# Kernel tuning notes

Measured on AMD Instinct MI355X. Metric: run time of the kernel, lower is better.

## Reference

```python
import jax, jax.numpy as jnp
import numpy as np

DEPTH, EMBED, HEADS, FF = 4, 512, 8, 2048
POS_SCALE, POS_WEIGHT = 0.1, 1.0
EPS = 1e-5  # torch LayerNorm default


def setup_inputs() -> dict:
    key = jax.random.key(0)
    ks = jax.random.split(key, 6)
    B, L = 8, 1024
    s = 0.02
    x = jax.random.normal(ks[0], (B, L, EMBED), jnp.float32)
    Wqkv = jax.random.normal(ks[1], (DEPTH, 3 * EMBED, EMBED), jnp.float32) * s
    bqkv = jnp.zeros((DEPTH, 3 * EMBED), jnp.float32)
    W1 = jax.random.normal(ks[2], (DEPTH, FF, EMBED), jnp.float32) * s
    b1 = jnp.zeros((DEPTH, FF), jnp.float32)
    W2 = jax.random.normal(ks[3], (DEPTH, EMBED, FF), jnp.float32) * s
    b2 = jnp.zeros((DEPTH, EMBED), jnp.float32)
    g = jnp.ones((DEPTH, EMBED), jnp.float32)
    bt = jnp.zeros((DEPTH, EMBED), jnp.float32)
    return {"input": x, "Wqkv": Wqkv, "bqkv": bqkv, "W1": W1, "b1": b1,
            "W2": W2, "b2": b2, "g1": g, "bt1": bt, "g2": g, "bt2": bt,
            "g3": g, "bt3": bt}


def _ln(x, g, b):
    m = x.mean(-1, keepdims=True)
    v = ((x - m) ** 2).mean(-1, keepdims=True)
    return (x - m) * jax.lax.rsqrt(v + EPS) * g + b


def reference(input, Wqkv, bqkv, W1, b1, W2, b2, g1, bt1, g2, bt2, g3, bt3):
    x = input
    B, L, E = x.shape
    hd = E // HEADS
    pos_idx = jnp.arange(L)
    # additive relative-position bias: exp(-|i-j| * scale) * weight
    pos = jnp.exp(-jnp.abs(pos_idx[:, None] - pos_idx[None, :]).astype(x.dtype) * POS_SCALE) * POS_WEIGHT
    triu = jnp.triu(jnp.ones((L, L), dtype=bool), 1)
    inv_sqrt_hd = jnp.asarray(1.0 / np.sqrt(hd), x.dtype)
    for d in range(DEPTH):
        # --- RelativeMultiheadAttention self-attn block ---
        qkv = jnp.einsum('ble,fe->blf', x, Wqkv[d]) + bqkv[d]
        q = qkv[..., :E].reshape(B, L, HEADS, hd).transpose(0, 2, 1, 3)
        k = qkv[..., E:2 * E].reshape(B, L, HEADS, hd).transpose(0, 2, 1, 3)
        logits = jnp.einsum('bhqd,bhkd->bhqk', q, k) * inv_sqrt_hd
        # nn.MultiheadAttention returns head-AVERAGED softmax weights
        A = jax.nn.softmax(logits, axis=-1).mean(axis=1)  # [B,L,L]
        # torch: attn_logits[triu(attn_logits,1).to(bool)] = -inf (nonzero strict upper)
        A = jnp.where(triu & (A != 0), -jnp.inf, A)
        W = jax.nn.softmax(A + pos[None], axis=-1)
        sa = jnp.einsum('bqk,bke->bqe', W, x)  # value is RAW x (no v-proj/out-proj)
        x = _ln(x + sa, g1[d], bt1[d])
        # --- NoopAttention cross-attn block contributes zeros ---
        x = _ln(x, g2[d], bt2[d])
        # --- FFN block (relu activation, post-norm) ---
        h = jax.nn.relu(jnp.einsum('ble,fe->blf', x, W1[d]) + b1[d])
        ff = jnp.einsum('blf,ef->ble', h, W2[d]) + b2[d]
        x = _ln(x + ff, g3[d], bt3[d])
    return x
```

## Files before the change

### kernel.cpp

```cpp
#include <hip/hip_runtime.h>

#define NB 8
#define SEQ 1024
#define EMB 512
#define FFD 2048
#define NROWS (NB*SEQ)
#define LNEPS 1e-5f

typedef __bf16 bf16x8 __attribute__((ext_vector_type(8)));
typedef float f32x4 __attribute__((ext_vector_type(4)));

__device__ __forceinline__ unsigned short f2bf(float f){
  unsigned u = __builtin_bit_cast(unsigned, f);
  u += 0x7fffu + ((u>>16)&1u);
  return (unsigned short)(u>>16);
}
__device__ __forceinline__ bf16x8 ld_bf8(const unsigned short* p){
  return *(const bf16x8*)p;
}
__device__ __forceinline__ void async_copy16(const void* g, void* l){
  __builtin_amdgcn_global_load_lds((const __attribute__((address_space(1))) unsigned int*)g,
                                   (__attribute__((address_space(3))) unsigned int*)l,
                                   16, 0, 0);
}

__device__ __forceinline__ float2 block_sum2(float a,float b){
  #pragma unroll
  for(int k=32;k>=1;k>>=1){ a += __shfl_xor(a,k,64); b += __shfl_xor(b,k,64); }
  __shared__ float sa[4], sb[4];
  int w = threadIdx.x>>6;
  __syncthreads();
  if((threadIdx.x&63)==0){ sa[w]=a; sb[w]=b; }
  __syncthreads();
  return make_float2(sa[0]+sa[1]+sa[2]+sa[3], sb[0]+sb[1]+sb[2]+sb[3]);
}

template<bool OUTBF16, bool RELU, bool BIAS, bool CAUSAL, int NT>
__global__ __launch_bounds__(256,4) void gemm_db(
    const unsigned short* __restrict__ Ag, const unsigned short* __restrict__ Bg,
    const float* __restrict__ bias, void* __restrict__ Cg,
    int K, int lda, int ldb, int ldc,
    long long strA, long long strB, long long strC)
{
  constexpr int NJ = NT/32;
  __shared__ unsigned short As[2][128*32];
  __shared__ unsigned short Bs[2][NT*32];
  const unsigned short* Ab = Ag + blockIdx.z*strA;
  const unsigned short* Bb = Bg + blockIdx.z*strB;
  const int m0 = blockIdx.y*128, n0 = blockIdx.x*NT;
  const int t = threadIdx.x;
  const int lane = t & 63, w = t >> 6;
  const int wy = w >> 1, wx = w & 1;
  const int q = lane >> 4, c = lane & 15;
  f32x4 acc[4][NJ] = {};
  const int kend = CAUSAL ? (m0 + 128) : K;
  const int srow = t >> 2;
  const int sk = (t & 3) * 8;
  const int gk = ((t & 3) ^ ((t >> 3) & 3)) * 8;
  const int rs = (q ^ ((c >> 1) & 3)) * 8;

#define STAGE(bi, kk) do { \
    async_copy16(Ab + (long long)(m0 + srow)*lda + (kk) + gk,      &As[bi][srow*32 + sk]); \
    async_copy16(Ab + (long long)(m0 + srow + 64)*lda + (kk) + gk, &As[bi][(srow+64)*32 + sk]); \
    async_copy16(Bb + (long long)(n0 + srow)*ldb + (kk) + gk,      &Bs[bi][srow*32 + sk]); \
    if(NT == 128) \
      async_copy16(Bb + (long long)(n0 + srow + 64)*ldb + (kk) + gk, &Bs[bi][(srow+64)*32 + sk]); \
  } while(0)

  STAGE(0, 0);
  int buf = 0;
  for(int k0 = 0; k0 < kend; k0 += 32, buf ^= 1){
    __syncthreads();
    if(k0 + 32 < kend) STAGE(buf^1, k0 + 32);
    bf16x8 af[4], bfr[NJ];
    #pragma unroll
    for(int fi=0; fi<4; fi++) af[fi]  = ld_bf8(&As[buf][(wy*64 + fi*16 + c)*32 + rs]);
    #pragma unroll
    for(int fj=0; fj<NJ; fj++) bfr[fj] = ld_bf8(&Bs[buf][(wx*(NT/2) + fj*16 + c)*32 + rs]);
    #pragma unroll
    for(int fi=0; fi<4; fi++)
      #pragma unroll
      for(int fj=0; fj<NJ; fj++)
        acc[fi][fj] = __builtin_amdgcn_mfma_f32_16x16x32_bf16(af[fi], bfr[fj], acc[fi][fj], 0,0,0);
  }
#undef STAGE
  #pragma unroll
  for(int fi=0; fi<4; fi++){
    #pragma unroll
    for(int fj=0; fj<NJ; fj++){
      const int row = m0 + wy*64 + fi*16 + q*4;
      const int col = n0 + wx*(NT/2) + fj*16 + c;
      const float bv = (BIAS && blockIdx.z==0) ? bias[col] : 0.f;
      #pragma unroll
      for(int r=0; r<4; r++){
        float v = acc[fi][fj][r] + bv;
        if(RELU) v = fmaxf(v, 0.f);
        long long off = blockIdx.z*strC + (long long)(row+r)*ldc + col;
        if(OUTBF16) ((unsigned short*)Cg)[off] = f2bf(v);
        else        ((float*)Cg)[off] = v;
      }
    }
  }
}

__global__ __launch_bounds__(256) void qk_dsum(
    const unsigned short* __restrict__ qkv, float* __restrict__ dsum)
{
  __shared__ unsigned short As[128*32];
  __shared__ unsigned short Bs[128*32];
  const int bh = blockIdx.z, b = bh >> 3, h = bh & 7;
  const int i0 = blockIdx.y*128, j0 = blockIdx.x*128;
  const unsigned short* Ab = qkv + (long long)b*SEQ*1024 + h*64;
  const unsigned short* Bb = qkv + (long long)b*SEQ*1024 + 512 + h*64;
  const int t = threadIdx.x, lane = t & 63, w = t >> 6;
  const int wy = w >> 1, wx = w & 1, q = lane >> 4, c = lane & 15;
  f32x4 acc[4][4] = {};
  const int srow = t >> 2;
  const int sk = (t & 3) * 8;
  const int gk = ((t & 3) ^ ((t >> 3) & 3)) * 8;
  const int rs = (q ^ ((c >> 1) & 3)) * 8;
  #pragma unroll
  for(int k0 = 0; k0 < 64; k0 += 32){
    async_copy16(Ab + (long long)(i0 + srow)*1024 + k0 + gk,      As + srow*32 + sk);
    async_copy16(Ab + (long long)(i0 + srow + 64)*1024 + k0 + gk, As + (srow+64)*32 + sk);
    async_copy16(Bb + (long long)(j0 + srow)*1024 + k0 + gk,      Bs + srow*32 + sk);
    async_copy16(Bb + (long long)(j0 + srow + 64)*1024 + k0 + gk, Bs + (srow+64)*32 + sk);
    __syncthreads();
    bf16x8 af[4], bfr[4];
    #pragma unroll
    for(int fi=0; fi<4; fi++) af[fi]  = ld_bf8(As + (wy*64 + fi*16 + c)*32 + rs);
    #pragma unroll
    for(int fj=0; fj<4; fj++) bfr[fj] = ld_bf8(Bs + (wx*64 + fj*16 + c)*32 + rs);
    #pragma unroll
    for(int fi=0; fi<4; fi++)
      #pragma unroll
      for(int fj=0; fj<4; fj++)
        acc[fi][fj] = __builtin_amdgcn_mfma_f32_16x16x32_bf16(af[fi], bfr[fj], acc[fi][fj], 0,0,0);
    __syncthreads();
  }
  #pragma unroll
  for(int fi=0; fi<4; fi++){
    #pragma unroll
    for(int r=0; r<4; r++){
      float s = 0.f;
      #pragma unroll
      for(int fj=0; fj<4; fj++) s += __expf(acc[fi][fj][r]*0.125f);
      s += __shfl_xor(s,1,64); s += __shfl_xor(s,2,64);
      s += __shfl_xor(s,4,64); s += __shfl_xor(s,8,64);
      if(c == 0)
        atomicAdd(&dsum[(long long)bh*SEQ + i0 + wy*64 + fi*16 + q*4 + r], s);
    }
  }
}

__global__ __launch_bounds__(256) void attn_w(
    const unsigned short* __restrict__ qkv, const float* __restrict__ dsum,
    unsigned short* __restrict__ Wm, float* __restrict__ Dsum2)
{
  __shared__ unsigned short As[64*32];
  __shared__ unsigned short Bs[64*32];
  __shared__ float inv8[8][64];
  const int b = blockIdx.y;
  int x = blockIdx.x;
  int it = 0;
  while((it+1)*(it+2)/2 <= x) ++it;
  const int jt = x - it*(it+1)/2;
  const int i0 = it*64, j0 = jt*64;
  const int t = threadIdx.x, lane = t & 63, w = t >> 6;
  const int q = lane >> 4, c = lane & 15;
  for(int u = t; u < 512; u += 256){
    int h = u >> 6, r = u & 63;
    inv8[h][r] = 1.f/(8.f*dsum[((long long)(b*8 + h))*SEQ + i0 + r]);
  }
  const unsigned short* Qb = qkv + (long long)b*SEQ*1024;
  const int srow = t >> 2;
  const int sk = (t & 3) * 8;
  const int gk = ((t & 3) ^ ((t >> 3) & 3)) * 8;
  const int rs = (q ^ ((c >> 1) & 3)) * 8;
  f32x4 at[4] = {};
  for(int h = 0; h < 8; h++){
    f32x4 l[4] = {};
    #pragma unroll
    for(int k0 = 0; k0 < 64; k0 += 32){
      __syncthreads();
      async_copy16(Qb + (long long)(i0 + srow)*1024 + h*64 + k0 + gk,       As + srow*32 + sk);
      async_copy16(Qb + (long long)(j0 + srow)*1024 + 512 + h*64 + k0 + gk, Bs + srow*32 + sk);
      __syncthreads();
      bf16x8 af = ld_bf8(As + (w*16 + c)*32 + rs);
      bf16x8 bfr[4];
      #pragma unroll
      for(int fj=0; fj<4; fj++) bfr[fj] = ld_bf8(Bs + (fj*16 + c)*32 + rs);
      #pragma unroll
      for(int fj=0; fj<4; fj++)
        l[fj] = __builtin_amdgcn_mfma_f32_16x16x32_bf16(af, bfr[fj], l[fj], 0,0,0);
    }
    #pragma unroll
    for(int r=0; r<4; r++){
      float iv = inv8[h][w*16 + q*4 + r];
      #pragma unroll
      for(int fj=0; fj<4; fj++)
        at[fj][r] += __expf(l[fj][r]*0.125f)*iv;
    }
  }
  float Dacc[4] = {};
  #pragma unroll
  for(int fj=0; fj<4; fj++){
    #pragma unroll
    for(int r=0; r<4; r++){
      const int i = i0 + w*16 + q*4 + r;
      const int j = j0 + fj*16 + c;
      float wv = 0.f;
      if(j <= i) wv = __expf(at[fj][r] + __expf((float)(j - i)*0.1f));
      Wm[((long long)(b*SEQ + i))*SEQ + j] = f2bf(wv);
      Dacc[r] += wv;
    }
  }
  #pragma unroll
  for(int r=0; r<4; r++){
    Dacc[r] += __shfl_xor(Dacc[r],1,64); Dacc[r] += __shfl_xor(Dacc[r],2,64);
    Dacc[r] += __shfl_xor(Dacc[r],4,64); Dacc[r] += __shfl_xor(Dacc[r],8,64);
    if(c == 0)
      atomicAdd(&Dsum2[(long long)b*SEQ + i0 + w*16 + q*4 + r], Dacc[r]);
  }
}

__global__ __launch_bounds__(256) void transpose_bf16(
    const unsigned short* __restrict__ src, unsigned short* __restrict__ dst)
{
  __shared__ unsigned short tile[64*65];
  const int bx = blockIdx.x;
  const int by = blockIdx.y;
  const int t = threadIdx.x;
  #pragma unroll
  for(int p=0; p<2; p++){
    int idx = t + p*256;
    int r = idx >> 3, cc = (idx & 7)*8;
    alignas(16) unsigned short e[8];
    *(uint4*)e = *(const uint4*)(src + (long long)(by*64 + r)*512 + bx*64 + cc);
    #pragma unroll
    for(int u=0; u<8; u++) tile[r*65 + cc + u] = e[u];
  }
  __syncthreads();
  #pragma unroll
  for(int p=0; p<2; p++){
    int idx = t + p*256;
    int r2 = idx >> 3, c2 = (idx & 7)*8;
    alignas(16) unsigned short e[8];
    #pragma unroll
    for(int u=0; u<8; u++) e[u] = tile[(c2+u)*65 + r2];
    *(uint4*)(dst + (long long)(bx*64 + r2)*8192 + by*64 + c2) = *(const uint4*)e;
  }
}

__global__ __launch_bounds__(256) void residual_ln2(
    const float* __restrict__ X, const float* __restrict__ SA,
    const float* __restrict__ Dsum2,
    const float* __restrict__ g1, const float* __restrict__ b1,
    const float* __restrict__ g2, const float* __restrict__ b2,
    float* __restrict__ XO, unsigned short* __restrict__ Xb)
{
  const long long row = blockIdx.x;
  const int t = threadIdx.x;
  const float s = 1.f/Dsum2[row];
  float v0 = X[row*EMB + t]       + SA[row*EMB + t]*s;
  float v1 = X[row*EMB + t + 256] + SA[row*EMB + t + 256]*s;
  float2 ss = block_sum2(v0+v1, v0*v0+v1*v1);
  float mean = ss.x*(1.f/EMB);
  float var  = ss.y*(1.f/EMB) - mean*mean;
  float rstd = rsqrtf(var + LNEPS);
  float y0 = (v0-mean)*rstd*g1[t]     + b1[t];
  float y1 = (v1-mean)*rstd*g1[t+256] + b1[t+256];
  ss = block_sum2(y0+y1, y0*y0+y1*y1);
  mean = ss.x*(1.f/EMB);
  var  = ss.y*(1.f/EMB) - mean*mean;
  rstd = rsqrtf(var + LNEPS);
  float o0 = (y0-mean)*rstd*g2[t]     + b2[t];
  float o1 = (y1-mean)*rstd*g2[t+256] + b2[t+256];
  XO[row*EMB + t] = o0;       XO[row*EMB + t + 256] = o1;
  Xb[row*EMB + t] = f2bf(o0); Xb[row*EMB + t + 256] = f2bf(o1);
}

__global__ __launch_bounds__(256) void residual_ln(
    const float* __restrict__ X, const float* __restrict__ R1,
    const float* __restrict__ R2,
    const float* __restrict__ g, const float* __restrict__ b,
    float* __restrict__ XO, unsigned short* __restrict__ Xb)
{
  const long long row = blockIdx.x;
  const int t = threadIdx.x;
  float v0 = X[row*EMB + t]       + R1[row*EMB + t]       + R2[row*EMB + t];
  float v1 = X[row*EMB + t + 256] + R1[row*EMB + t + 256] + R2[row*EMB + t + 256];
  float2 ss = block_sum2(v0+v1, v0*v0+v1*v1);
  float mean = ss.x*(1.f/EMB);
  float var  = ss.y*(1.f/EMB) - mean*mean;
  float rstd = rsqrtf(var + LNEPS);
  float o0 = (v0-mean)*rstd*g[t]     + b[t];
  float o1 = (v1-mean)*rstd*g[t+256] + b[t+256];
  XO[row*EMB + t] = o0;       XO[row*EMB + t + 256] = o1;
  Xb[row*EMB + t] = f2bf(o0); Xb[row*EMB + t + 256] = f2bf(o1);
}

__global__ __launch_bounds__(256) void init_x(
    const float* __restrict__ in, float* __restrict__ XO,
    unsigned short* __restrict__ Xb)
{
  const long long row = blockIdx.x;
  const int t = threadIdx.x;
  float v0 = in[row*EMB + t];
  float v1 = in[row*EMB + t + 256];
  XO[row*EMB + t] = v0;       XO[row*EMB + t + 256] = v1;
  Xb[row*EMB + t] = f2bf(v0); Xb[row*EMB + t + 256] = f2bf(v1);
}

__global__ __launch_bounds__(256) void cvt_bf16(
    const float* __restrict__ src, unsigned short* __restrict__ dst, long long n)
{
  long long i = ((long long)blockIdx.x*256 + threadIdx.x)*4;
  if(i < n){
    float4 v = *(const float4*)(src + i);
    ushort4 o = make_ushort4(f2bf(v.x), f2bf(v.y), f2bf(v.z), f2bf(v.w));
    *(ushort4*)(dst + i) = o;
  }
}

__global__ __launch_bounds__(256) void cvt_qkv(
    const float* __restrict__ src, unsigned short* __restrict__ dst)
{
  long long i = ((long long)blockIdx.x*256 + threadIdx.x)*4;
  int layer = (int)(i >> 19);
  long long within = i & ((1LL<<19)-1);
  float4 v = *(const float4*)(src + (long long)layer*1536*512 + within);
  ushort4 o = make_ushort4(f2bf(v.x), f2bf(v.y), f2bf(v.z), f2bf(v.w));
  *(ushort4*)(dst + i) = o;
}

extern "C" void kernel_launch(void* const* d_in, const int* in_sizes, int n_in,
                              void* d_out, int out_size, void* d_ws, size_t ws_size,
                              hipStream_t stream)
{
  const float* x_in = (const float*)d_in[0];
  const float* Wqkv = (const float*)d_in[1];
  const float* bqkv = (const float*)d_in[2];
  const float* W1   = (const float*)d_in[3];
  const float* b1   = (const float*)d_in[4];
  const float* W2   = (const float*)d_in[5];
  const float* b2   = (const float*)d_in[6];
  const float* g1   = (const float*)d_in[7];
  const float* bt1  = (const float*)d_in[8];
  const float* g2   = (const float*)d_in[9];
  const float* bt2  = (const float*)d_in[10];
  const float* g3   = (const float*)d_in[11];
  const float* bt3  = (const float*)d_in[12];

  float* X = (float*)d_out;

  char* ws = (char*)d_ws;
  unsigned short* qkv    = (unsigned short*)(ws);
  unsigned short* hbuf   = (unsigned short*)(ws + ((size_t)16<<20));
  unsigned short* Wm     = (unsigned short*)(ws + ((size_t)48<<20));
  float*          tmp    = (float*)         (ws + ((size_t)64<<20));
  float*          tmp2   = (float*)         (ws + ((size_t)80<<20));
  unsigned short* Xb     = (unsigned short*)(ws + ((size_t)96<<20));
  unsigned short* XT     = (unsigned short*)(ws + ((size_t)104<<20));
  unsigned short* Wqkvb  = (unsigned short*)(ws + ((size_t)112<<20));
  unsigned short* W1b    = (unsigned short*)(ws + ((size_t)118<<20));
  unsigned short* W2b    = (unsigned short*)(ws + ((size_t)126<<20));
  float*          dsum   = (float*)         (ws + ((size_t)134<<20));
  float*          Dsum2  = (float*)         (ws + ((size_t)134<<20) + (256<<10));

  cvt_qkv<<<2048, 256, 0, stream>>>(Wqkv, Wqkvb);
  cvt_bf16<<<4096, 256, 0, stream>>>(W1, W1b, (long long)4*FFD*EMB);
  cvt_bf16<<<4096, 256, 0, stream>>>(W2, W2b, (long long)4*EMB*FFD);
  init_x<<<NROWS, 256, 0, stream>>>(x_in, X, Xb);
  transpose_bf16<<<dim3(8,128), 256, 0, stream>>>(Xb, XT);

  for(int d=0; d<4; d++){
    hipMemsetAsync(dsum, 0, (256<<10) + (32<<10), stream);

    gemm_db<true,false,true,false,128><<<dim3(8, 64, 1), 256, 0, stream>>>(
        Xb, Wqkvb + (size_t)d*1024*EMB, bqkv + (size_t)d*1536, qkv,
        EMB, EMB, EMB, 1024, 0, 0, 0);

    qk_dsum<<<dim3(8, 8, 64), 256, 0, stream>>>(qkv, dsum);

    attn_w<<<dim3(136, NB), 256, 0, stream>>>(qkv, dsum, Wm, Dsum2);

    gemm_db<false,false,false,true,64><<<dim3(8, 8, NB), 256, 0, stream>>>(
        Wm, XT, nullptr, tmp,
        SEQ, SEQ, NROWS, EMB,
        (long long)SEQ*SEQ, 1024, (long long)SEQ*EMB);

    residual_ln2<<<NROWS, 256, 0, stream>>>(X, tmp, Dsum2,
        g1 + d*EMB, bt1 + d*EMB, g2 + d*EMB, bt2 + d*EMB, X, Xb);

    gemm_db<true,true,true,false,128><<<dim3(16, 64, 1), 256, 0, stream>>>(
        Xb, W1b + (size_t)d*FFD*EMB, b1 + (size_t)d*FFD, hbuf,
        EMB, EMB, EMB, FFD, 0, 0, 0);

    gemm_db<false,false,true,false,128><<<dim3(4, 64, 2), 256, 0, stream>>>(
        hbuf, W2b + (size_t)d*EMB*FFD, b2 + (size_t)d*EMB, tmp,
        1024, FFD, FFD, EMB,
        1024, 1024, (long long)NROWS*EMB);

    residual_ln<<<NROWS, 256, 0, stream>>>(X, tmp, tmp2,
        g3 + d*EMB, bt3 + d*EMB, X, Xb);
    transpose_bf16<<<dim3(8,128), 256, 0, stream>>>(Xb, XT);
  }
}
```

Measured before the change: 946.5 us.

## Remap GEMM tiles per XCD, replace atomics with partial sums, fuse weight casts

GEMM launches become 1D grids with a remap that hands each of the 8 XCDs (by block-id mod 8) a contiguous band of row tiles, so A-tile reuse stays inside one XCD's L2. The atomicAdd row-sum reductions in qk_dsum and attn_w are replaced by per-tile partial-sum buffers that later kernels add up, which also removes the per-layer memset. The three weight-conversion kernels are merged into one launch. The cost is extra reads of the partial sums in attn_w and residual_ln2, and index math at the start of every GEMM block.

```diff
diff --git a/kernel.cpp b/kernel.cpp
--- a/kernel.cpp
+++ b/kernel.cpp
@@ -40,14 +40,23 @@
     const unsigned short* __restrict__ Ag, const unsigned short* __restrict__ Bg,
     const float* __restrict__ bias, void* __restrict__ Cg,
     int K, int lda, int ldb, int ldc,
-    long long strA, long long strB, long long strC)
+    long long strA, long long strB, long long strC,
+    int rt, int ct)
 {
   constexpr int NJ = NT/32;
   __shared__ unsigned short As[2][128*32];
   __shared__ unsigned short Bs[2][NT*32];
-  const unsigned short* Ab = Ag + blockIdx.z*strA;
-  const unsigned short* Bb = Bg + blockIdx.z*strB;
-  const int m0 = blockIdx.y*128, n0 = blockIdx.x*NT;
+  const int id = blockIdx.x;
+  const int rc = rt*ct;
+  const int z  = id / rc;
+  const int rem = id - z*rc;
+  const int g = rem & 7, idx = rem >> 3;
+  const int rpg = rt >> 3;
+  const int row = g*rpg + (idx % rpg);
+  const int col = idx / rpg;
+  const unsigned short* Ab = Ag + z*strA;
+  const unsigned short* Bb = Bg + z*strB;
+  const int m0 = row*128, n0 = col*NT;
   const int t = threadIdx.x;
   const int lane = t & 63, w = t >> 6;
   const int wy = w >> 1, wx = w & 1;
@@ -88,14 +97,14 @@
   for(int fi=0; fi<4; fi++){
     #pragma unroll
     for(int fj=0; fj<NJ; fj++){
-      const int row = m0 + wy*64 + fi*16 + q*4;
-      const int col = n0 + wx*(NT/2) + fj*16 + c;
-      const float bv = (BIAS && blockIdx.z==0) ? bias[col] : 0.f;
+      const int crow = m0 + wy*64 + fi*16 + q*4;
+      const int ccol = n0 + wx*(NT/2) + fj*16 + c;
+      const float bv = (BIAS && z==0) ? bias[ccol] : 0.f;
       #pragma unroll
       for(int r=0; r<4; r++){
         float v = acc[fi][fj][r] + bv;
         if(RELU) v = fmaxf(v, 0.f);
-        long long off = blockIdx.z*strC + (long long)(row+r)*ldc + col;
+        long long off = z*strC + (long long)(crow+r)*ldc + ccol;
         if(OUTBF16) ((unsigned short*)Cg)[off] = f2bf(v);
         else        ((float*)Cg)[off] = v;
       }
@@ -104,10 +113,11 @@
 }
 
 __global__ __launch_bounds__(256) void qk_dsum(
-    const unsigned short* __restrict__ qkv, float* __restrict__ dsum)
+    const unsigned short* __restrict__ qkv, float* __restrict__ dpart)
 {
   __shared__ unsigned short As[128*32];
   __shared__ unsigned short Bs[128*32];
+  __shared__ float red[2][128];
   const int bh = blockIdx.z, b = bh >> 3, h = bh & 7;
   const int i0 = blockIdx.y*128, j0 = blockIdx.x*128;
   const unsigned short* Ab = qkv + (long long)b*SEQ*1024 + h*64;
@@ -147,15 +157,17 @@
       for(int fj=0; fj<4; fj++) s += __expf(acc[fi][fj][r]*0.125f);
       s += __shfl_xor(s,1,64); s += __shfl_xor(s,2,64);
       s += __shfl_xor(s,4,64); s += __shfl_xor(s,8,64);
-      if(c == 0)
-        atomicAdd(&dsum[(long long)bh*SEQ + i0 + wy*64 + fi*16 + q*4 + r], s);
+      if(c == 0) red[wx][wy*64 + fi*16 + q*4 + r] = s;
     }
   }
+  __syncthreads();
+  if(t < 128)
+    dpart[(((long long)blockIdx.x*NB + b)*8 + h)*SEQ + i0 + t] = red[0][t] + red[1][t];
 }
 
 __global__ __launch_bounds__(256) void attn_w(
-    const unsigned short* __restrict__ qkv, const float* __restrict__ dsum,
-    unsigned short* __restrict__ Wm, float* __restrict__ Dsum2)
+    const unsigned short* __restrict__ qkv, const float* __restrict__ dpart,
+    unsigned short* __restrict__ Wm, float* __restrict__ Dp)
 {
   __shared__ unsigned short As[64*32];
   __shared__ unsigned short Bs[64*32];
@@ -170,7 +182,11 @@
   const int q = lane >> 4, c = lane & 15;
   for(int u = t; u < 512; u += 256){
     int h = u >> 6, r = u & 63;
-    inv8[h][r] = 1.f/(8.f*dsum[((long long)(b*8 + h))*SEQ + i0 + r]);
+    float s = 0.f;
+    #pragma unroll
+    for(int j2 = 0; j2 < 8; j2++)
+      s += dpart[(((long long)j2*NB + b)*8 + h)*SEQ + i0 + r];
+    inv8[h][r] = 1.f/(8.f*s);
   }
   const unsigned short* Qb = qkv + (long long)b*SEQ*1024;
   const int srow = t >> 2;
@@ -220,7 +236,7 @@
     Dacc[r] += __shfl_xor(Dacc[r],1,64); Dacc[r] += __shfl_xor(Dacc[r],2,64);
     Dacc[r] += __shfl_xor(Dacc[r],4,64); Dacc[r] += __shfl_xor(Dacc[r],8,64);
     if(c == 0)
-      atomicAdd(&Dsum2[(long long)b*SEQ + i0 + w*16 + q*4 + r], Dacc[r]);
+      Dp[((long long)jt*NB + b)*SEQ + i0 + w*16 + q*4 + r] = Dacc[r];
   }
 }
 
@@ -254,14 +270,18 @@
 
 __global__ __launch_bounds__(256) void residual_ln2(
     const float* __restrict__ X, const float* __restrict__ SA,
-    const float* __restrict__ Dsum2,
+    const float* __restrict__ Dp,
     const float* __restrict__ g1, const float* __restrict__ b1,
     const float* __restrict__ g2, const float* __restrict__ b2,
     float* __restrict__ XO, unsigned short* __restrict__ Xb)
 {
   const long long row = blockIdx.x;
   const int t = threadIdx.x;
-  const float s = 1.f/Dsum2[row];
+  const int b = (int)(row >> 10), i = (int)(row & 1023), itile = i >> 6;
+  float Ds = 0.f;
+  for(int jt = 0; jt <= itile; jt++)
+    Ds += Dp[((long long)jt*NB + b)*SEQ + i];
+  const float s = 1.f/Ds;
   float v0 = X[row*EMB + t]       + SA[row*EMB + t]*s;
   float v1 = X[row*EMB + t + 256] + SA[row*EMB + t + 256]*s;
   float2 ss = block_sum2(v0+v1, v0*v0+v1*v1);
@@ -312,26 +332,30 @@
   Xb[row*EMB + t] = f2bf(v0); Xb[row*EMB + t + 256] = f2bf(v1);
 }
 
-__global__ __launch_bounds__(256) void cvt_bf16(
-    const float* __restrict__ src, unsigned short* __restrict__ dst, long long n)
-{
-  long long i = ((long long)blockIdx.x*256 + threadIdx.x)*4;
-  if(i < n){
-    float4 v = *(const float4*)(src + i);
-    ushort4 o = make_ushort4(f2bf(v.x), f2bf(v.y), f2bf(v.z), f2bf(v.w));
-    *(ushort4*)(dst + i) = o;
-  }
-}
-
-__global__ __launch_bounds__(256) void cvt_qkv(
-    const float* __restrict__ src, unsigned short* __restrict__ dst)
-{
-  long long i = ((long long)blockIdx.x*256 + threadIdx.x)*4;
-  int layer = (int)(i >> 19);
-  long long within = i & ((1LL<<19)-1);
-  float4 v = *(const float4*)(src + (long long)layer*1536*512 + within);
-  ushort4 o = make_ushort4(f2bf(v.x), f2bf(v.y), f2bf(v.z), f2bf(v.w));
-  *(ushort4*)(dst + i) = o;
+__global__ __launch_bounds__(256) void cvt_all(
+    const float* __restrict__ Wqkv, const float* __restrict__ W1,
+    const float* __restrict__ W2, unsigned short* __restrict__ Wqkvb,
+    unsigned short* __restrict__ W1b, unsigned short* __restrict__ W2b)
+{
+  const long long id = (long long)blockIdx.x*256 + threadIdx.x;
+  const long long n0 = 524288, n1 = 1048576;
+  float4 v; unsigned short* dst;
+  if(id < n0){
+    long long i = id*4;
+    int layer = (int)(i >> 19);
+    long long within = i & ((1LL<<19)-1);
+    v = *(const float4*)(Wqkv + (long long)layer*1536*512 + within);
+    dst = Wqkvb + i;
+  } else if(id < n0 + n1){
+    long long i = (id - n0)*4;
+    v = *(const float4*)(W1 + i);
+    dst = W1b + i;
+  } else {
+    long long i = (id - n0 - n1)*4;
+    v = *(const float4*)(W2 + i);
+    dst = W2b + i;
+  }
+  *(ushort4*)dst = make_ushort4(f2bf(v.x), f2bf(v.y), f2bf(v.z), f2bf(v.w));
 }
 
 extern "C" void kernel_launch(void* const* d_in, const int* in_sizes, int n_in,
@@ -365,42 +389,38 @@
   unsigned short* Wqkvb  = (unsigned short*)(ws + ((size_t)112<<20));
   unsigned short* W1b    = (unsigned short*)(ws + ((size_t)118<<20));
   unsigned short* W2b    = (unsigned short*)(ws + ((size_t)126<<20));
-  float*          dsum   = (float*)         (ws + ((size_t)134<<20));
-  float*          Dsum2  = (float*)         (ws + ((size_t)134<<20) + (256<<10));
-
-  cvt_qkv<<<2048, 256, 0, stream>>>(Wqkv, Wqkvb);
-  cvt_bf16<<<4096, 256, 0, stream>>>(W1, W1b, (long long)4*FFD*EMB);
-  cvt_bf16<<<4096, 256, 0, stream>>>(W2, W2b, (long long)4*EMB*FFD);
+  float*          dpart  = (float*)         (ws + ((size_t)134<<20));
+  float*          Dp     = (float*)         (ws + ((size_t)136<<20));
+
+  cvt_all<<<(524288 + 2*1048576)/256, 256, 0, stream>>>(Wqkv, W1, W2, Wqkvb, W1b, W2b);
   init_x<<<NROWS, 256, 0, stream>>>(x_in, X, Xb);
   transpose_bf16<<<dim3(8,128), 256, 0, stream>>>(Xb, XT);
 
   for(int d=0; d<4; d++){
-    hipMemsetAsync(dsum, 0, (256<<10) + (32<<10), stream);
-
-    gemm_db<true,false,true,false,128><<<dim3(8, 64, 1), 256, 0, stream>>>(
+    gemm_db<true,false,true,false,128><<<dim3(512), 256, 0, stream>>>(
         Xb, Wqkvb + (size_t)d*1024*EMB, bqkv + (size_t)d*1536, qkv,
-        EMB, EMB, EMB, 1024, 0, 0, 0);
-
-    qk_dsum<<<dim3(8, 8, 64), 256, 0, stream>>>(qkv, dsum);
-
-    attn_w<<<dim3(136, NB), 256, 0, stream>>>(qkv, dsum, Wm, Dsum2);
-
-    gemm_db<false,false,false,true,64><<<dim3(8, 8, NB), 256, 0, stream>>>(
+        EMB, EMB, EMB, 1024, 0, 0, 0, 64, 8);
+
+    qk_dsum<<<dim3(8, 8, 64), 256, 0, stream>>>(qkv, dpart);
+
+    attn_w<<<dim3(136, NB), 256, 0, stream>>>(qkv, dpart, Wm, Dp);
+
+    gemm_db<false,false,false,true,64><<<dim3(512), 256, 0, stream>>>(
         Wm, XT, nullptr, tmp,
         SEQ, SEQ, NROWS, EMB,
-        (long long)SEQ*SEQ, 1024, (long long)SEQ*EMB);
-
-    residual_ln2<<<NROWS, 256, 0, stream>>>(X, tmp, Dsum2,
+        (long long)SEQ*SEQ, 1024, (long long)SEQ*EMB, 8, 8);
+
+    residual_ln2<<<NROWS, 256, 0, stream>>>(X, tmp, Dp,
         g1 + d*EMB, bt1 + d*EMB, g2 + d*EMB, bt2 + d*EMB, X, Xb);
 
-    gemm_db<true,true,true,false,128><<<dim3(16, 64, 1), 256, 0, stream>>>(
+    gemm_db<true,true,true,false,128><<<dim3(1024), 256, 0, stream>>>(
         Xb, W1b + (size_t)d*FFD*EMB, b1 + (size_t)d*FFD, hbuf,
-        EMB, EMB, EMB, FFD, 0, 0, 0);
-
-    gemm_db<false,false,true,false,128><<<dim3(4, 64, 2), 256, 0, stream>>>(
+        EMB, EMB, EMB, FFD, 0, 0, 0, 64, 16);
+
+    gemm_db<false,false,true,false,128><<<dim3(512), 256, 0, stream>>>(
         hbuf, W2b + (size_t)d*EMB*FFD, b2 + (size_t)d*EMB, tmp,
         1024, FFD, FFD, EMB,
-        1024, 1024, (long long)NROWS*EMB);
+        1024, 1024, (long long)NROWS*EMB, 64, 4);
 
     residual_ln<<<NROWS, 256, 0, stream>>>(X, tmp, tmp2,
         g3 + d*EMB, bt3 + d*EMB, X, Xb);
```

Result: no change. 947.7 us (+0.1%).
